# Performance work log

Hardware: AMD Instinct MI355X
Metric: run time of the kernel (lower is better)

## Reference

```python
import jax, jax.numpy as jnp
import numpy as np

N = 50000
E = 800000
D_IN, D_HID, D_OUT = 256, 256, 128


def _xavier(key, shape):
    fan_in, fan_out = shape
    limit = float(np.sqrt(6.0 / (fan_in + fan_out)))
    return jax.random.uniform(key, shape, jnp.float32, -limit, limit)


def setup_inputs() -> dict:
    key = jax.random.key(0)
    ks = jax.random.split(key, 12)
    x = jax.random.normal(ks[0], (N, D_IN), jnp.float32)
    edge_index = jax.random.randint(ks[1], (2, E), 0, N, dtype=jnp.int64)
    batch = jnp.zeros((N,), jnp.int64)
    # per-layer: message weight W, linear weight LW (stored [in, out]), bias b
    w1 = _xavier(ks[2], (D_IN, D_HID))
    lw1 = _xavier(ks[3], (D_IN, D_HID))
    lb1 = jnp.zeros((D_HID,), jnp.float32)
    w2 = _xavier(ks[4], (D_HID, D_HID))
    lw2 = _xavier(ks[5], (D_HID, D_HID))
    lb2 = jnp.zeros((D_HID,), jnp.float32)
    w3 = _xavier(ks[6], (D_HID, D_OUT))
    lw3 = _xavier(ks[7], (D_HID, D_OUT))
    lb3 = jnp.zeros((D_OUT,), jnp.float32)
    return {"x": x, "edge_index": edge_index, "batch": batch,
            "w1": w1, "lw1": lw1, "lb1": lb1,
            "w2": w2, "lw2": lw2, "lb2": lb2,
            "w3": w3, "lw3": lw3, "lb3": lb3}


def _gcn_layer(x, W, LW, b, row, col, norm):
    # message: norm * (x_j @ W); equivalent and cheaper: transform nodes once, gather
    xw = x @ W                                   # [N, out]
    msg = norm[:, None] * xw[row]                # [E, out]
    agg = jax.ops.segment_sum(msg, col, num_segments=x.shape[0])  # scatter-add at col
    return agg + x @ LW + b                      # residual linear path


def reference(x, edge_index, batch, w1, lw1, lb1, w2, lw2, lb2, w3, lw3, lb3):
    row, col = edge_index[0], edge_index[1]
    ones = jnp.ones((row.shape[0],), x.dtype)
    out_deg = jax.ops.segment_sum(ones, row, num_segments=N)
    in_deg = jax.ops.segment_sum(ones, col, num_segments=N)
    # inf at zero-degree nodes never gets gathered (those nodes have no edges)
    norm = out_deg[row] ** -0.5 * in_deg[col] ** -0.5  # [E]

    h = jax.nn.relu(_gcn_layer(x, w1, lw1, lb1, row, col, norm))
    h = jax.nn.relu(_gcn_layer(h, w2, lw2, lb2, row, col, norm))
    h = jax.nn.sigmoid(_gcn_layer(h, w3, lw3, lb3, row, col, norm))
    return h
```

## Files before the change

### kernel.cpp

```cpp
#include <hip/hip_runtime.h>
#include <hip/hip_bf16.h>
#include <math.h>

#define NNODES 50000
#define NEDGES 800000
#define HNB 128
#define HBINS 50176
#define SCAN_NB 196

typedef short s8v __attribute__((ext_vector_type(8)));
typedef float f4v __attribute__((ext_vector_type(4)));
typedef unsigned int u32;
using bf16 = __hip_bfloat16;

static __device__ __forceinline__ float bflo(unsigned int x) {
    union { unsigned int i; float f; } c; c.i = x << 16; return c.f;
}
static __device__ __forceinline__ float bfhi(unsigned int x) {
    union { unsigned int i; float f; } c; c.i = x & 0xffff0000u; return c.f;
}
static __device__ __forceinline__ void fma8(float* a, float w, uint4 q) {
    a[0] += w * bflo(q.x); a[1] += w * bfhi(q.x);
    a[2] += w * bflo(q.y); a[3] += w * bfhi(q.y);
    a[4] += w * bflo(q.z); a[5] += w * bfhi(q.z);
    a[6] += w * bflo(q.w); a[7] += w * bfhi(q.w);
}
static __device__ __forceinline__ void gld_lds16(const void* g, void* l) {
    __builtin_amdgcn_global_load_lds((const __attribute__((address_space(1))) u32*)g,
                                     (__attribute__((address_space(3))) u32*)l, 16, 0, 0);
}


__global__ void k_packbt(const float* __restrict__ W, const float* __restrict__ LW,
                         bf16* __restrict__ out, int CC) {
    int i = blockIdx.x * blockDim.x + threadIdx.x;
    if (i >= CC * 512) return;
    int n = i / 512, k = i % 512;
    float v = (k < 256) ? W[k * CC + n] : LW[(k - 256) * CC + n];
    out[i] = __float2bfloat16(v);
}


__global__ void k_f2b_strided(const float* __restrict__ x, ushort* __restrict__ gh) {
    int i = blockIdx.x * blockDim.x + threadIdx.x;
    if (i >= NNODES * 64) return;
    int v = i >> 6, c = (i & 63) * 4;
    float4 f = *(const float4*)(x + (size_t)v * 256 + c);
    union { bf16 h[4]; uint2 u; } o;
    o.h[0] = __float2bfloat16(f.x); o.h[1] = __float2bfloat16(f.y);
    o.h[2] = __float2bfloat16(f.z); o.h[3] = __float2bfloat16(f.w);
    *(uint2*)(gh + (size_t)v * 512 + 256 + c) = o.u;
}


__global__ __launch_bounds__(256) void k_hist(const int* __restrict__ ei, ushort* __restrict__ partials) {
    __shared__ unsigned int h32[HBINS / 2];
    int b = blockIdx.x, row = blockIdx.y, t = threadIdx.x;
    for (int i = t; i < HBINS / 2; i += 256) h32[i] = 0;
    __syncthreads();
    const int chunk = NEDGES / HNB;
    int beg = b * chunk, end = beg + chunk;
    const int* p = ei + (size_t)row * NEDGES;
    for (int e = beg + t; e < end; e += 256) {
        int id = p[e];
        atomicAdd(&h32[id >> 1], 1u << (16 * (id & 1)));
    }
    __syncthreads();
    unsigned int* o32 = (unsigned int*)(partials + ((size_t)row * HNB + b) * HBINS);
    for (int i = t; i < HBINS / 2; i += 256) o32[i] = h32[i];
}

__global__ __launch_bounds__(256) void k_hist_reduce(const ushort* __restrict__ partials,
                                                     float* __restrict__ rsqrt_out,
                                                     int* __restrict__ in_cnt,
                                                     int* __restrict__ block_sums) {
    __shared__ int sm[256];
    int row = blockIdx.y;
    int i = blockIdx.x * 256 + threadIdx.x;
    const ushort* p = partials + (size_t)row * HNB * HBINS + i;
    int s = 0;
#pragma unroll 4
    for (int b = 0; b < HNB; ++b) s += p[(size_t)b * HBINS];
    if (row == 0) {
        if (i < NNODES) rsqrt_out[i] = rsqrtf((float)s);
    } else {
        if (i < NNODES) in_cnt[i] = s;
        sm[threadIdx.x] = s;
        __syncthreads();
        for (int off = 128; off > 0; off >>= 1) {
            if (threadIdx.x < off) sm[threadIdx.x] += sm[threadIdx.x + off];
            __syncthreads();
        }
        if (threadIdx.x == 0) block_sums[blockIdx.x] = sm[0];
    }
}


__global__ void k_scan_blocks(const int* __restrict__ block_sums, int* __restrict__ block_base, int nb) {
    __shared__ int s[256];
    int t = threadIdx.x;
    int v = (t < nb) ? block_sums[t] : 0;
    s[t] = v;
    __syncthreads();
    for (int off = 1; off < 256; off <<= 1) {
        int u = (t >= off) ? s[t - off] : 0;
        __syncthreads();
        s[t] += u;
        __syncthreads();
    }
    block_base[t] = s[t] - v;
}

__global__ void k_scan_final(const int* __restrict__ in_cnt, const int* __restrict__ block_base,
                             int* __restrict__ offsets, int* __restrict__ cursor) {
    __shared__ int s[256];
    int b = blockIdx.x, t = threadIdx.x;
    int i = b * 256 + t;
    int v = (i < NNODES) ? in_cnt[i] : 0;
    s[t] = v;
    __syncthreads();
    for (int off = 1; off < 256; off <<= 1) {
        int u = (t >= off) ? s[t - off] : 0;
        __syncthreads();
        s[t] += u;
        __syncthreads();
    }
    int excl = s[t] - v + block_base[b];
    if (i < NNODES) { offsets[i] = excl; cursor[i] = excl; }
    if (i == NNODES - 1) offsets[NNODES] = excl + v;
}

__global__ void k_scatter(const int* __restrict__ ei, const float* __restrict__ rsqrt_out,
                          int* __restrict__ cursor, int2* __restrict__ edge_sw) {
    int e = blockIdx.x * blockDim.x + threadIdx.x;
    if (e < NEDGES) {
        int r = ei[e], c = ei[NEDGES + e];
        int p = atomicAdd(&cursor[c], 1);
        edge_sw[p] = make_int2(r, __float_as_int(rsqrt_out[r]));
    }
}

__global__ __launch_bounds__(256) void k_gather(const ushort* __restrict__ hsrc,
                                                const int* __restrict__ offsets,
                                                const int2* __restrict__ edge_sw,
                                                ushort* __restrict__ Gdst) {
    int lane = threadIdx.x & 63;
    int v = blockIdx.x * 32 + (threadIdx.x >> 6) * 8 + (lane >> 3);
    if (v >= NNODES) return;
    int sl = lane & 7;
    int col0 = blockIdx.y * 64;

    int beg = offsets[v], end = offsets[v + 1];
    float a0[8], a1[8];
#pragma unroll
    for (int c = 0; c < 8; ++c) { a0[c] = 0.f; a1[c] = 0.f; }

    const ushort* base = hsrc + col0 + sl * 8;
    int j = beg;
    for (; j + 2 <= end; j += 2) {
        int2 e0 = edge_sw[j];
        int2 e1 = edge_sw[j + 1];
        uint4 q0 = *(const uint4*)(base + (size_t)e0.x * 512);
        uint4 q1 = *(const uint4*)(base + (size_t)e1.x * 512);
        fma8(a0, __int_as_float(e0.y), q0);
        fma8(a1, __int_as_float(e1.y), q1);
    }
    if (j < end) {
        int2 e0 = edge_sw[j];
        uint4 q0 = *(const uint4*)(base + (size_t)e0.x * 512);
        fma8(a0, __int_as_float(e0.y), q0);
    }
    float sc = (end > beg) ? rsqrtf((float)(end - beg)) : 0.f;
    union { bf16 h[8]; uint4 u; } o;
#pragma unroll
    for (int c = 0; c < 8; ++c) o.h[c] = __float2bfloat16((a0[c] + a1[c]) * sc);
    *(uint4*)(Gdst + (size_t)v * 512 + col0 + sl * 8) = o.u;
}

template<int CC, int OST, int OOFF, int ACT>
__global__ __launch_bounds__(256) void k_gemm(const ushort* __restrict__ A,
                                              const bf16* __restrict__ Bt,
                                              const float* __restrict__ bias,
                                              void* __restrict__ Out) {
    __shared__ bf16 As[128 * 32];
    __shared__ bf16 Bs[128 * 32];
    int t = threadIdx.x;
    int wave = t >> 6, lane = t & 63;
    int r0 = blockIdx.x * 128;
    int n0 = blockIdx.y * 128;
    int wr = wave >> 1, wc = wave & 1;

    f4v acc[4][4];
#pragma unroll
    for (int i = 0; i < 4; ++i)
#pragma unroll
        for (int j = 0; j < 4; ++j) acc[i][j] = (f4v){0.f, 0.f, 0.f, 0.f};

    const char* Ab = (const char*)A;
    const char* Bb = (const char*)Bt;
    for (int k0 = 0; k0 < 512; k0 += 32) {
#pragma unroll
        for (int r = 0; r < 2; ++r) {
            int o = r * 4096 + wave * 1024 + lane * 16;
            int row = o >> 6, kb = o & 63;
            if (r0 + row < NNODES)
                gld_lds16(Ab + (size_t)(r0 + row) * 1024 + k0 * 2 + kb, (char*)As + o);
            gld_lds16(Bb + (size_t)(n0 + row) * 1024 + k0 * 2 + kb, (char*)Bs + o);
        }
        __syncthreads();
        int ml = lane & 15, kq = (lane >> 4) * 8;
        s8v a[4], b[4];
#pragma unroll
        for (int i = 0; i < 4; ++i)
            a[i] = *(const s8v*)&As[(wr * 64 + i * 16 + ml) * 32 + kq];
#pragma unroll
        for (int j = 0; j < 4; ++j)
            b[j] = *(const s8v*)&Bs[(wc * 64 + j * 16 + ml) * 32 + kq];
#pragma unroll
        for (int i = 0; i < 4; ++i)
#pragma unroll
            for (int j = 0; j < 4; ++j)
                acc[i][j] = __builtin_amdgcn_mfma_f32_16x16x32_bf16(a[i], b[j], acc[i][j], 0, 0, 0);
        __syncthreads();
    }
    int ml = lane & 15, q4 = (lane >> 4) * 4;
#pragma unroll
    for (int i = 0; i < 4; ++i) {
#pragma unroll
        for (int rr = 0; rr < 4; ++rr) {
            int grow = r0 + wr * 64 + i * 16 + q4 + rr;
            if (grow < NNODES) {
#pragma unroll
                for (int j = 0; j < 4; ++j) {
                    int gcol = n0 + wc * 64 + j * 16 + ml;
                    float vv = acc[i][j][rr] + bias[gcol];
                    if (ACT == 1) {
                        ((ushort*)Out)[(size_t)grow * OST + OOFF + gcol] =
                            __bfloat16_as_ushort(__float2bfloat16(fmaxf(vv, 0.f)));
                    } else {
                        ((float*)Out)[(size_t)grow * OST + gcol] = 1.f / (1.f + expf(-vv));
                    }
                }
            }
        }
    }
}


extern "C" void kernel_launch(void* const* d_in, const int* in_sizes, int n_in,
                              void* d_out, int out_size, void* d_ws, size_t ws_size,
                              hipStream_t stream) {
    const float* x   = (const float*)d_in[0];
    const int*   ei  = (const int*)d_in[1];
    const float* w1  = (const float*)d_in[3];
    const float* lw1 = (const float*)d_in[4];
    const float* lb1 = (const float*)d_in[5];
    const float* w2  = (const float*)d_in[6];
    const float* lw2 = (const float*)d_in[7];
    const float* lb2 = (const float*)d_in[8];
    const float* w3  = (const float*)d_in[9];
    const float* lw3 = (const float*)d_in[10];
    const float* lb3 = (const float*)d_in[11];
    float* out = (float*)d_out;

    char* ws = (char*)d_ws;
    size_t off = 0;
    auto alloc = [&](size_t bytes) -> void* {
        void* p = ws + off;
        off += (bytes + 255) & ~(size_t)255;
        return p;
    };
    int*    in_cnt     = (int*)alloc((size_t)HBINS * 4);
    float*  rsqrt_out  = (float*)alloc((size_t)HBINS * 4);
    int*    offsets    = (int*)alloc((size_t)(NNODES + 1) * 4);
    int*    cursor     = (int*)alloc((size_t)NNODES * 4);
    int*    block_sums = (int*)alloc((size_t)256 * 4);
    int*    block_base = (int*)alloc((size_t)256 * 4);
    ushort* partials   = (ushort*)alloc((size_t)2 * HNB * HBINS * 2);
    int2*   edge_sw    = (int2*)alloc((size_t)NEDGES * 8);
    bf16*   wt1        = (bf16*)alloc((size_t)256 * 512 * 2);
    bf16*   wt2        = (bf16*)alloc((size_t)256 * 512 * 2);
    bf16*   wt3        = (bf16*)alloc((size_t)128 * 512 * 2);
    ushort* ghA        = (ushort*)alloc((size_t)NNODES * 512 * 2);
    ushort* ghB        = (ushort*)alloc((size_t)NNODES * 512 * 2);

    k_packbt<<<512, 256, 0, stream>>>(w1, lw1, wt1, 256);
    k_packbt<<<512, 256, 0, stream>>>(w2, lw2, wt2, 256);
    k_packbt<<<256, 256, 0, stream>>>(w3, lw3, wt3, 128);
    k_f2b_strided<<<(NNODES * 64 + 255) / 256, 256, 0, stream>>>(x, ghA);

    k_hist<<<dim3(HNB, 2), 256, 0, stream>>>(ei, partials);
    k_hist_reduce<<<dim3(SCAN_NB, 2), 256, 0, stream>>>(partials, rsqrt_out, in_cnt, block_sums);
    k_scan_blocks<<<1, 256, 0, stream>>>(block_sums, block_base, SCAN_NB);
    k_scan_final<<<SCAN_NB, 256, 0, stream>>>(in_cnt, block_base, offsets, cursor);
    k_scatter<<<(NEDGES + 255) / 256, 256, 0, stream>>>(ei, rsqrt_out, cursor, edge_sw);

    dim3 ggrid((NNODES + 31) / 32, 4);
    int gx = (NNODES + 127) / 128;

    k_gather<<<ggrid, 256, 0, stream>>>(ghA + 256, offsets, edge_sw, ghA);
    k_gemm<256, 512, 256, 1><<<dim3(gx, 2), 256, 0, stream>>>(ghA, wt1, lb1, ghB);
    k_gather<<<ggrid, 256, 0, stream>>>(ghB + 256, offsets, edge_sw, ghB);
    k_gemm<256, 512, 256, 1><<<dim3(gx, 2), 256, 0, stream>>>(ghB, wt2, lb2, ghA);
    k_gather<<<ggrid, 256, 0, stream>>>(ghA + 256, offsets, edge_sw, ghA);
    k_gemm<128, 128, 0, 2><<<dim3(gx, 1), 256, 0, stream>>>(ghA, wt3, lb3, out);
}
```

Measured before the change: 466.2 us.

## Reorder layer 3 to transform before aggregating and widen GEMM tiles to full output width

For the last layer, nodes are first multiplied by W3 (256->128) and the narrower 128-wide features are then gathered, instead of gathering 256-wide features. This halves the edge-gather traffic for that layer. The residual GEMM then adds the fp32 aggregate inside its epilogue. The GEMM kernel also now computes the full output width per block (128x256 tiles), so each A tile is loaded once, at the cost of more accumulator registers per thread. The change adds an extra GEMM launch and an fp32 intermediate buffer.

```diff
diff --git a/kernel.cpp b/kernel.cpp
--- a/kernel.cpp
+++ b/kernel.cpp
@@ -29,7 +29,6 @@
     __builtin_amdgcn_global_load_lds((const __attribute__((address_space(1))) u32*)g,
                                      (__attribute__((address_space(3))) u32*)l, 16, 0, 0);
 }
-
 
 __global__ void k_packbt(const float* __restrict__ W, const float* __restrict__ LW,
                          bf16* __restrict__ out, int CC) {
@@ -38,6 +37,12 @@
     int n = i / 512, k = i % 512;
     float v = (k < 256) ? W[k * CC + n] : LW[(k - 256) * CC + n];
     out[i] = __float2bfloat16(v);
+}
+__global__ void k_packt(const float* __restrict__ W, bf16* __restrict__ out) {
+    int i = blockIdx.x * blockDim.x + threadIdx.x;
+    if (i >= 128 * 256) return;
+    int n = i / 256, k = i % 256;
+    out[i] = __float2bfloat16(W[k * 128 + n]);
 }
 
 
@@ -140,10 +145,11 @@
     }
 }
 
+template<int SST, int OFP32>
 __global__ __launch_bounds__(256) void k_gather(const ushort* __restrict__ hsrc,
                                                 const int* __restrict__ offsets,
                                                 const int2* __restrict__ edge_sw,
-                                                ushort* __restrict__ Gdst) {
+                                                void* __restrict__ Gdst) {
     int lane = threadIdx.x & 63;
     int v = blockIdx.x * 32 + (threadIdx.x >> 6) * 8 + (lane >> 3);
     if (v >= NNODES) return;
@@ -160,66 +166,78 @@
     for (; j + 2 <= end; j += 2) {
         int2 e0 = edge_sw[j];
         int2 e1 = edge_sw[j + 1];
-        uint4 q0 = *(const uint4*)(base + (size_t)e0.x * 512);
-        uint4 q1 = *(const uint4*)(base + (size_t)e1.x * 512);
+        uint4 q0 = *(const uint4*)(base + (size_t)e0.x * SST);
+        uint4 q1 = *(const uint4*)(base + (size_t)e1.x * SST);
         fma8(a0, __int_as_float(e0.y), q0);
         fma8(a1, __int_as_float(e1.y), q1);
     }
     if (j < end) {
         int2 e0 = edge_sw[j];
-        uint4 q0 = *(const uint4*)(base + (size_t)e0.x * 512);
+        uint4 q0 = *(const uint4*)(base + (size_t)e0.x * SST);
         fma8(a0, __int_as_float(e0.y), q0);
     }
     float sc = (end > beg) ? rsqrtf((float)(end - beg)) : 0.f;
-    union { bf16 h[8]; uint4 u; } o;
-#pragma unroll
-    for (int c = 0; c < 8; ++c) o.h[c] = __float2bfloat16((a0[c] + a1[c]) * sc);
-    *(uint4*)(Gdst + (size_t)v * 512 + col0 + sl * 8) = o.u;
-}
-
-template<int CC, int OST, int OOFF, int ACT>
-__global__ __launch_bounds__(256) void k_gemm(const ushort* __restrict__ A,
-                                              const bf16* __restrict__ Bt,
-                                              const float* __restrict__ bias,
-                                              void* __restrict__ Out) {
+    if (OFP32) {
+        float* op = (float*)Gdst + (size_t)v * 128 + col0 + sl * 8;
+        *(float4*)op = (float4){(a0[0]+a1[0])*sc, (a0[1]+a1[1])*sc, (a0[2]+a1[2])*sc, (a0[3]+a1[3])*sc};
+        *(float4*)(op+4) = (float4){(a0[4]+a1[4])*sc, (a0[5]+a1[5])*sc, (a0[6]+a1[6])*sc, (a0[7]+a1[7])*sc};
+    } else {
+        union { bf16 h[8]; uint4 u; } o;
+#pragma unroll
+        for (int c = 0; c < 8; ++c) o.h[c] = __float2bfloat16((a0[c] + a1[c]) * sc);
+        *(uint4*)((ushort*)Gdst + (size_t)v * 512 + col0 + sl * 8) = o.u;
+    }
+}
+
+template<int CC, int KK, int ACT>
+__global__ __launch_bounds__(256) void k_gemm_w(const ushort* __restrict__ A, int AST,
+                                                const bf16* __restrict__ Bt,
+                                                const float* __restrict__ bias,
+                                                const float* __restrict__ G3,
+                                                void* __restrict__ Out, int OST, int OOFF) {
     __shared__ bf16 As[128 * 32];
-    __shared__ bf16 Bs[128 * 32];
+    __shared__ bf16 Bs[CC * 32];
+    const int NT = CC / 32;
     int t = threadIdx.x;
     int wave = t >> 6, lane = t & 63;
     int r0 = blockIdx.x * 128;
-    int n0 = blockIdx.y * 128;
     int wr = wave >> 1, wc = wave & 1;
 
-    f4v acc[4][4];
+    f4v acc[4][NT];
 #pragma unroll
     for (int i = 0; i < 4; ++i)
 #pragma unroll
-        for (int j = 0; j < 4; ++j) acc[i][j] = (f4v){0.f, 0.f, 0.f, 0.f};
+        for (int j = 0; j < NT; ++j) acc[i][j] = (f4v){0.f, 0.f, 0.f, 0.f};
 
     const char* Ab = (const char*)A;
     const char* Bb = (const char*)Bt;
-    for (int k0 = 0; k0 < 512; k0 += 32) {
+    for (int k0 = 0; k0 < KK; k0 += 32) {
 #pragma unroll
         for (int r = 0; r < 2; ++r) {
             int o = r * 4096 + wave * 1024 + lane * 16;
             int row = o >> 6, kb = o & 63;
             if (r0 + row < NNODES)
-                gld_lds16(Ab + (size_t)(r0 + row) * 1024 + k0 * 2 + kb, (char*)As + o);
-            gld_lds16(Bb + (size_t)(n0 + row) * 1024 + k0 * 2 + kb, (char*)Bs + o);
+                gld_lds16(Ab + ((size_t)(r0 + row) * AST + k0) * 2 + kb, (char*)As + o);
         }
+#pragma unroll
+        for (int r = 0; r < CC / 64; ++r) {
+            int o = r * 4096 + wave * 1024 + lane * 16;
+            int row = o >> 6, kb = o & 63;
+            gld_lds16(Bb + ((size_t)row * KK + k0) * 2 + kb, (char*)Bs + o);
+        }
         __syncthreads();
         int ml = lane & 15, kq = (lane >> 4) * 8;
-        s8v a[4], b[4];
+        s8v a[4], b[NT];
 #pragma unroll
         for (int i = 0; i < 4; ++i)
             a[i] = *(const s8v*)&As[(wr * 64 + i * 16 + ml) * 32 + kq];
 #pragma unroll
-        for (int j = 0; j < 4; ++j)
-            b[j] = *(const s8v*)&Bs[(wc * 64 + j * 16 + ml) * 32 + kq];
+        for (int j = 0; j < NT; ++j)
+            b[j] = *(const s8v*)&Bs[(wc * (CC / 2) + j * 16 + ml) * 32 + kq];
 #pragma unroll
         for (int i = 0; i < 4; ++i)
 #pragma unroll
-            for (int j = 0; j < 4; ++j)
+            for (int j = 0; j < NT; ++j)
                 acc[i][j] = __builtin_amdgcn_mfma_f32_16x16x32_bf16(a[i], b[j], acc[i][j], 0, 0, 0);
         __syncthreads();
     }
@@ -231,13 +249,18 @@
             int grow = r0 + wr * 64 + i * 16 + q4 + rr;
             if (grow < NNODES) {
 #pragma unroll
-                for (int j = 0; j < 4; ++j) {
-                    int gcol = n0 + wc * 64 + j * 16 + ml;
-                    float vv = acc[i][j][rr] + bias[gcol];
-                    if (ACT == 1) {
+                for (int j = 0; j < NT; ++j) {
+                    int gcol = wc * (CC / 2) + j * 16 + ml;
+                    float vv = acc[i][j][rr];
+                    if (ACT == 0) {
+                        ((ushort*)Out)[(size_t)grow * OST + OOFF + gcol] =
+                            __bfloat16_as_ushort(__float2bfloat16(vv));
+                    } else if (ACT == 1) {
+                        vv += bias[gcol];
                         ((ushort*)Out)[(size_t)grow * OST + OOFF + gcol] =
                             __bfloat16_as_ushort(__float2bfloat16(fmaxf(vv, 0.f)));
                     } else {
+                        vv += bias[gcol] + G3[(size_t)grow * 128 + gcol];
                         ((float*)Out)[(size_t)grow * OST + gcol] = 1.f / (1.f + expf(-vv));
                     }
                 }
@@ -280,13 +303,17 @@
     int2*   edge_sw    = (int2*)alloc((size_t)NEDGES * 8);
     bf16*   wt1        = (bf16*)alloc((size_t)256 * 512 * 2);
     bf16*   wt2        = (bf16*)alloc((size_t)256 * 512 * 2);
-    bf16*   wt3        = (bf16*)alloc((size_t)128 * 512 * 2);
+    bf16*   wt3a       = (bf16*)alloc((size_t)128 * 256 * 2);
+    bf16*   wt3b       = (bf16*)alloc((size_t)128 * 256 * 2);
     ushort* ghA        = (ushort*)alloc((size_t)NNODES * 512 * 2);
     ushort* ghB        = (ushort*)alloc((size_t)NNODES * 512 * 2);
+    ushort* xw3        = (ushort*)alloc((size_t)NNODES * 128 * 2);
+    float*  G3         = (float*)alloc((size_t)NNODES * 128 * 4);
 
     k_packbt<<<512, 256, 0, stream>>>(w1, lw1, wt1, 256);
     k_packbt<<<512, 256, 0, stream>>>(w2, lw2, wt2, 256);
-    k_packbt<<<256, 256, 0, stream>>>(w3, lw3, wt3, 128);
+    k_packt<<<128, 256, 0, stream>>>(w3, wt3a);
+    k_packt<<<128, 256, 0, stream>>>(lw3, wt3b);
     k_f2b_strided<<<(NNODES * 64 + 255) / 256, 256, 0, stream>>>(x, ghA);
 
     k_hist<<<dim3(HNB, 2), 256, 0, stream>>>(ei, partials);
@@ -295,13 +322,15 @@
     k_scan_final<<<SCAN_NB, 256, 0, stream>>>(in_cnt, block_base, offsets, cursor);
     k_scatter<<<(NEDGES + 255) / 256, 256, 0, stream>>>(ei, rsqrt_out, cursor, edge_sw);
 
-    dim3 ggrid((NNODES + 31) / 32, 4);
+    dim3 g4((NNODES + 31) / 32, 4);
+    dim3 g2((NNODES + 31) / 32, 2);
     int gx = (NNODES + 127) / 128;
 
-    k_gather<<<ggrid, 256, 0, stream>>>(ghA + 256, offsets, edge_sw, ghA);
-    k_gemm<256, 512, 256, 1><<<dim3(gx, 2), 256, 0, stream>>>(ghA, wt1, lb1, ghB);
-    k_gather<<<ggrid, 256, 0, stream>>>(ghB + 256, offsets, edge_sw, ghB);
-    k_gemm<256, 512, 256, 1><<<dim3(gx, 2), 256, 0, stream>>>(ghB, wt2, lb2, ghA);
-    k_gather<<<ggrid, 256, 0, stream>>>(ghA + 256, offsets, edge_sw, ghA);
-    k_gemm<128, 128, 0, 2><<<dim3(gx, 1), 256, 0, stream>>>(ghA, wt3, lb3, out);
-}
+    k_gather<512, 0><<<g4, 256, 0, stream>>>(ghA + 256, offsets, edge_sw, ghA);
+    k_gemm_w<256, 512, 1><<<gx, 256, 0, stream>>>(ghA, 512, wt1, lb1, nullptr, ghB, 512, 256);
+    k_gather<512, 0><<<g4, 256, 0, stream>>>(ghB + 256, offsets, edge_sw, ghB);
+    k_gemm_w<256, 512, 1><<<gx, 256, 0, stream>>>(ghB, 512, wt2, lb2, nullptr, ghA, 512, 256);
+    k_gemm_w<128, 256, 0><<<gx, 256, 0, stream>>>(ghA + 256, 512, wt3a, nullptr, nullptr, xw3, 128, 0);
+    k_gather<128, 1><<<g2, 256, 0, stream>>>(xw3, offsets, edge_sw, G3);
+    k_gemm_w<128, 256, 2><<<gx, 256, 0, stream>>>(ghA + 256, 512, wt3b, lb3, G3, out, 128, 0);
+}
```

Result: slower. 476.5 us (+2.2%).
